# Kernel optimization log

Measured on AMD Instinct MI355X. Metric: run time of the kernel, lower is better.

Reference implementation:

```python
import jax, jax.numpy as jnp
import numpy as np

HEAD, SIZE = 16, 64
DIM = HEAD * SIZE
NINF = -10000.0
EPS = 1e-6


def setup_inputs() -> dict:
    key = jax.random.key(0)
    ks = jax.random.split(key, 12)
    B, S = 4, 2048
    std = 0.02
    return {
        "x": jax.random.normal(ks[0], (B, S, DIM), jnp.float32),
        "mask": jax.random.randint(ks[1], (B, S), 0, 2, jnp.int32),
        "wq_w": jax.random.normal(ks[2], (DIM, DIM), jnp.float32) * std,
        "wq_b": jnp.zeros((DIM,), jnp.float32),
        "wk_w": jax.random.normal(ks[3], (DIM, DIM), jnp.float32) * std,
        "wk_b": jnp.zeros((DIM,), jnp.float32),
        "wv_w": jax.random.normal(ks[4], (DIM, DIM), jnp.float32) * std,
        "wv_b": jnp.zeros((DIM,), jnp.float32),
        "dense_w": jax.random.normal(ks[5], (DIM, DIM), jnp.float32) * std,
        "dense_b": jnp.zeros((DIM,), jnp.float32),
        "gamma": jnp.ones((DIM,), jnp.float32),
        "beta": jnp.zeros((DIM,), jnp.float32),
    }


def _split_heads(t):
    # [B, S, DIM] -> [B, H, S, size]
    B, S, _ = t.shape
    return t.reshape(B, S, HEAD, SIZE).transpose(0, 2, 1, 3)


def _layernorm(x, gamma, beta):
    mu = jnp.mean(x, axis=-1, keepdims=True)
    var = jnp.mean(jnp.square(x - mu), axis=-1, keepdims=True)
    return (x - mu) * jax.lax.rsqrt(var + EPS) * gamma + beta


def reference(x, mask, wq_w, wq_b, wk_w, wk_b, wv_w, wv_b, dense_w, dense_b, gamma, beta):
    B, S, _ = x.shape
    q = _split_heads(x @ wq_w + wq_b)
    k = _split_heads(x @ wk_w + wk_b)
    v = _split_heads(x @ wv_w + wv_b)
    # scores [B, H, S, S]
    scores = jnp.einsum("bhqd,bhkd->bhqk", q, k) / jnp.sqrt(jnp.float32(SIZE))
    scores = scores + mask.astype(jnp.float32)[:, None, None, :] * NINF
    attn = jax.nn.softmax(scores, axis=-1)
    ctx = jnp.einsum("bhqk,bhkd->bhqd", attn, v)  # [B, H, S, size]
    ctx = ctx.transpose(0, 2, 1, 3).reshape(B, S, DIM)
    out = _layernorm(x + (ctx @ dense_w + dense_b), gamma, beta)
    return out, attn
```

## Files before the change

### kernel.cpp

```cpp
#include <hip/hip_runtime.h>
#include <stdint.h>

#define NB 4
#define NS 2048
#define NH 16
#define HSZ 64
#define ND 1024
#define NM (NB*NS)
#define QSCALE 0.180336880f
#define MADD2 -14426.950409f

typedef unsigned short u16;
typedef unsigned int u32;
typedef __attribute__((ext_vector_type(4))) float f32x4;
typedef __attribute__((ext_vector_type(8))) __bf16 bf16x8;

static __device__ __forceinline__ u16 f2bf(float f){
  unsigned int x = __builtin_bit_cast(unsigned int, f);
  x += 0x7fffu + ((x >> 16) & 1u);
  return (u16)(x >> 16);
}
static __device__ __forceinline__ u16 f2bf_rz(float f){
  return (u16)(__builtin_bit_cast(unsigned int, f) >> 16);
}

#define GLDS16(gp, lp) __builtin_amdgcn_global_load_lds( \
    (const __attribute__((address_space(1))) void*)(gp),  \
    (__attribute__((address_space(3))) void*)(lp), 16, 0, 0)

__global__ __launch_bounds__(256) void k_cast(const float4* __restrict__ in,
                                              ushort4* __restrict__ out, int n4){
  int i = blockIdx.x*256 + threadIdx.x;
  if (i >= n4) return;
  float4 v = in[i];
  ushort4 o;
  o.x = f2bf(v.x); o.y = f2bf(v.y); o.z = f2bf(v.z); o.w = f2bf(v.w);
  out[i] = o;
}

__global__ __launch_bounds__(256) void k_transpose4(const float* __restrict__ wq,
    const float* __restrict__ wk, const float* __restrict__ wv,
    const float* __restrict__ wd, u16* __restrict__ wcat, u16* __restrict__ wdt){
  __shared__ float t[32][33];
  const int z = blockIdx.z;
  const float* in = (z==0) ? wq : (z==1) ? wk : (z==2) ? wv : wd;
  u16* out = (z<3) ? (wcat + (size_t)z*ND*ND) : wdt;
  int tx = threadIdx.x & 31, ty = threadIdx.x >> 5;
  int n0 = blockIdx.x*32, k0 = blockIdx.y*32;
  #pragma unroll
  for (int i=0;i<32;i+=8)
    t[ty+i][tx] = in[(size_t)(k0+ty+i)*ND + n0 + tx];
  __syncthreads();
  #pragma unroll
  for (int i=0;i<32;i+=8)
    out[(size_t)(n0+ty+i)*ND + k0 + tx] = f2bf(t[tx][ty+i]);
}

template<int EPI>
__global__ __launch_bounds__(256,2) void k_gemm(const u16* __restrict__ A,
    const u16* __restrict__ Bt, const float* __restrict__ b0,
    const float* __restrict__ b1, const float* __restrict__ b2,
    const float* __restrict__ resid, u16* __restrict__ Qo, u16* __restrict__ Ko,
    u16* __restrict__ Vto, float* __restrict__ Out){
  __shared__ u16 sAB[2][128*64];
  u16* sA = sAB[0];
  u16* sB = sAB[1];
  const int tid = threadIdx.x;
  const int wave = tid >> 6, lane = tid & 63;
  const int l15 = lane & 15, l4 = lane >> 4;
  const int m0 = blockIdx.x * 128, n0 = blockIdx.y * 128;
  const int wm = wave >> 1, wn = wave & 1;
  const f32x4 vz = {0.f,0.f,0.f,0.f};
  f32x4 acc[4][4];
  #pragma unroll
  for (int i=0;i<4;i++)
    #pragma unroll
    for (int j=0;j<4;j++) acc[i][j] = vz;

  for (int k0 = 0; k0 < 1024; k0 += 64){
    __syncthreads();
    #pragma unroll
    for (int t=0; t<4; t++){
      const int jb = (t*4 + wave)*64;
      const int j  = jb + lane;
      const int r = j >> 3, c = (j & 7) << 3;
      GLDS16(A  + (((size_t)(m0 + r)) << 10) + (size_t)(k0 + c), sA + jb*8);
      GLDS16(Bt + (((size_t)(n0 + r)) << 10) + (size_t)(k0 + c), sB + jb*8);
    }
    __syncthreads();
    #pragma unroll
    for (int kk=0; kk<64; kk+=32){
      bf16x8 af[4], bv[4];
      #pragma unroll
      for (int mi=0;mi<4;mi++)
        af[mi] = *(const bf16x8*)(const void*)(sA + (wm*64 + mi*16 + l15)*64 + kk + l4*8);
      #pragma unroll
      for (int ni=0;ni<4;ni++)
        bv[ni] = *(const bf16x8*)(const void*)(sB + (wn*64 + ni*16 + l15)*64 + kk + l4*8);
      #pragma unroll
      for (int mi=0;mi<4;mi++)
        #pragma unroll
        for (int ni=0;ni<4;ni++)
          acc[mi][ni] = __builtin_amdgcn_mfma_f32_16x16x32_bf16(af[mi], bv[ni], acc[mi][ni], 0, 0, 0);
    }
  }

  if (EPI == 0){
    const int sec = n0 >> 10;
    const float* bias = (sec==0) ? b0 : (sec==1) ? b1 : b2;
    const float scale = (sec==0) ? QSCALE : 1.0f;
    if (sec < 2){
      u16* dst = (sec==0) ? Qo : Ko;
      #pragma unroll
      for (int mi=0;mi<4;mi++){
        #pragma unroll
        for (int ni=0;ni<4;ni++){
          const int n = n0 + wn*64 + ni*16 + l15;
          const int nn = n & (ND-1);
          const int h = nn >> 6, d = nn & 63;
          const float bvv = bias[nn];
          #pragma unroll
          for (int j=0;j<4;j++){
            const int m = m0 + wm*64 + mi*16 + l4*4 + j;
            const int b = m >> 11, s = m & (NS-1);
            const float v = (acc[mi][ni][j] + bvv) * scale;
            dst[((((size_t)b*NH + h)*NS + s) << 6) + d] = f2bf(v);
          }
        }
      }
    } else {
      __syncthreads();
      u16 (*sT)[128] = (u16(*)[128])sAB;
      #pragma unroll
      for (int mi=0;mi<4;mi++){
        #pragma unroll
        for (int ni=0;ni<4;ni++){
          const int nl = wn*64 + ni*16 + l15;
          const float bvv = bias[(n0 & (ND-1)) + nl];
          #pragma unroll
          for (int j=0;j<4;j++){
            const int ml = wm*64 + mi*16 + l4*4 + j;
            sT[nl][ml] = f2bf(acc[mi][ni][j] + bvv);
          }
        }
      }
      __syncthreads();
      const int nbase = n0 & (ND-1);
      const int b2 = m0 >> 11;
      const int sbase = m0 & (NS-1);
      #pragma unroll
      for (int it=0; it<8; ++it){
        const int idx = it*256 + tid;
        const int row = idx >> 4;
        const int ch  = (idx & 15) << 3;
        const int nn2 = nbase + row;
        const int h2 = nn2 >> 6, d2 = nn2 & 63;
        *(int4*)(void*)(Vto + ((((size_t)b2*NH + h2)*HSZ + d2) << 11) + sbase + ch)
            = *(const int4*)(const void*)&sT[row][ch];
      }
    }
  } else {
    #pragma unroll
    for (int mi=0;mi<4;mi++){
      #pragma unroll
      for (int ni=0;ni<4;ni++){
        const int n = n0 + wn*64 + ni*16 + l15;
        const float bvv = b0[n];
        #pragma unroll
        for (int j=0;j<4;j++){
          const int m = m0 + wm*64 + mi*16 + l4*4 + j;
          const size_t o = ((size_t)m << 10) + n;
          Out[o] = acc[mi][ni][j] + bvv + resid[o];
        }
      }
    }
  }
}

static __device__ __forceinline__ void attn_decode(int bid, int& qb, int& bh){
  const int x = bid & 7, t = bid >> 3;
  qb = t & 15;
  bh = (t >> 4) * 8 + x;
}
static __device__ __forceinline__ void attn_decode8(int bid, int& qb, int& bh){
  const int x = bid & 7, t = bid >> 3;
  qb = t & 7;
  bh = (t >> 3) * 8 + x;
}

__global__ __launch_bounds__(512,4) void k_attn_stats(const u16* __restrict__ Q,
    const u16* __restrict__ K, const int* __restrict__ mask,
    float* __restrict__ stats){
  __shared__ u16 sK[2][64][72];
  __shared__ float sMadd[NS];
  const int tid = threadIdx.x, wave = tid>>6, lane = tid&63;
  const int l15 = lane&15, l4 = lane>>4;
  int qb, bh; attn_decode8(blockIdx.x, qb, bh);
  const int b = bh >> 4;
  const size_t hoff = (size_t)bh * NS * HSZ;
  const int q0 = qb*256 + wave*32;
  const u16* Kg = K + hoff;
  bf16x8 qf0[2], qf1[2];
  #pragma unroll
  for (int m=0;m<2;m++){
    qf0[m] = *(const bf16x8*)(const void*)(Q + hoff + (size_t)(q0+m*16+l15)*HSZ + l4*8);
    qf1[m] = *(const bf16x8*)(const void*)(Q + hoff + (size_t)(q0+m*16+l15)*HSZ + 32 + l4*8);
  }
  const f32x4 vz = {0.f,0.f,0.f,0.f};
  const int r = tid >> 3, c = (tid & 7) << 3;
  float lr[2][4] = {{0.f,0.f,0.f,0.f},{0.f,0.f,0.f,0.f}};

  #pragma unroll
  for (int t=0;t<4;t++){
    const int kk = t*512 + tid;
    sMadd[kk] = mask[b*NS + kk] ? MADD2 : 0.f;
  }
  int4 rK = *(const int4*)(const void*)(Kg + (size_t)r*HSZ + c);
  *(int4*)(void*)&sK[0][r][c] = rK;
  rK = *(const int4*)(const void*)(Kg + (size_t)(64+r)*HSZ + c);
  __syncthreads();

  for (int kb=0; kb<NS; kb+=64){
    const int cur = (kb>>6)&1;
    if (kb+64 < NS)
      *(int4*)(void*)&sK[cur^1][r][c] = rK;
    if (kb+128 < NS)
      rK = *(const int4*)(const void*)(Kg + (size_t)(kb+128+r)*HSZ + c);
    #pragma unroll
    for (int n=0;n<4;n++){
      bf16x8 kf0 = *(const bf16x8*)(const void*)&sK[cur][n*16+l15][l4*8];
      bf16x8 kf1 = *(const bf16x8*)(const void*)&sK[cur][n*16+l15][32+l4*8];
      const float madd = sMadd[kb + n*16 + l15];
      #pragma unroll
      for (int m=0;m<2;m++){
        f32x4 a = vz;
        a = __builtin_amdgcn_mfma_f32_16x16x32_bf16(qf0[m], kf0, a, 0,0,0);
        a = __builtin_amdgcn_mfma_f32_16x16x32_bf16(qf1[m], kf1, a, 0,0,0);
        #pragma unroll
        for (int j=0;j<4;j++)
          lr[m][j] += __builtin_amdgcn_exp2f(a[j] + madd);
      }
    }
    __syncthreads();
  }
  #pragma unroll
  for (int m=0;m<2;m++)
    #pragma unroll
    for (int j=0;j<4;j++){
      float l = lr[m][j];
      #pragma unroll
      for (int off=1; off<16; off<<=1)
        l += __shfl_xor(l, off, 64);
      if (l15 == 0)
        stats[(size_t)bh*NS + q0 + m*16 + l4*4 + j] = 1.f/l;
    }
}

__global__ __launch_bounds__(512,4) void k_attn_pv(const u16* __restrict__ Q,
    const u16* __restrict__ K, const u16* __restrict__ Vt,
    const int* __restrict__ mask, const float* __restrict__ stats,
    float* __restrict__ attn, u16* __restrict__ ctx){
  __shared__ u16 sK[2][64][72];
  __shared__ u16 sV[2][64][72];
  __shared__ u16 sP[8][16][72];
  __shared__ float sMadd[NS];
  const int tid = threadIdx.x, wave = tid>>6, lane = tid&63;
  const int l15 = lane&15, l4 = lane>>4;
  int qb, bh; attn_decode(blockIdx.x, qb, bh);
  const int b = bh >> 4, h = bh & 15;
  const size_t hoff = (size_t)bh * NS * HSZ;
  const int q0 = qb*128 + wave*16;
  const u16* Kg = K + hoff;
  const u16* Vg = Vt + hoff;
  const bf16x8 qf0 = *(const bf16x8*)(const void*)(Q + hoff + (size_t)(q0+l15)*HSZ + l4*8);
  const bf16x8 qf1 = *(const bf16x8*)(const void*)(Q + hoff + (size_t)(q0+l15)*HSZ + 32 + l4*8);
  float rinv[4];
  #pragma unroll
  for (int j=0;j<4;j++)
    rinv[j] = stats[(size_t)bh*NS + q0 + l4*4 + j];
  const f32x4 vz = {0.f,0.f,0.f,0.f};
  f32x4 cacc[4];
  #pragma unroll
  for (int i=0;i<4;i++) cacc[i] = vz;
  float* attn_base = attn + (size_t)bh * NS * NS;
  const int r = tid >> 3, c = (tid & 7) << 3;

  #pragma unroll
  for (int t=0;t<4;t++){
    const int kk = t*512 + tid;
    sMadd[kk] = mask[b*NS + kk] ? MADD2 : 0.f;
  }
  int4 rK = *(const int4*)(const void*)(Kg + (size_t)r*HSZ + c);
  int4 rV = *(const int4*)(const void*)(Vg + (size_t)r*NS + c);
  *(int4*)(void*)&sK[0][r][c] = rK;
  *(int4*)(void*)&sV[0][r][c] = rV;
  rK = *(const int4*)(const void*)(Kg + (size_t)(64+r)*HSZ + c);
  rV = *(const int4*)(const void*)(Vg + (size_t)r*NS + 64 + c);
  __syncthreads();

  for (int kb=0; kb<NS; kb+=64){
    const int cur = (kb>>6)&1;
    if (kb+64 < NS){
      *(int4*)(void*)&sK[cur^1][r][c] = rK;
      *(int4*)(void*)&sV[cur^1][r][c] = rV;
    }
    if (kb+128 < NS){
      rK = *(const int4*)(const void*)(Kg + (size_t)(kb+128+r)*HSZ + c);
      rV = *(const int4*)(const void*)(Vg + (size_t)r*NS + (kb+128) + c);
    }
    #pragma unroll
    for (int n=0;n<4;n++){
      bf16x8 kf0 = *(const bf16x8*)(const void*)&sK[cur][n*16+l15][l4*8];
      bf16x8 kf1 = *(const bf16x8*)(const void*)&sK[cur][n*16+l15][32+l4*8];
      f32x4 a = vz;
      a = __builtin_amdgcn_mfma_f32_16x16x32_bf16(qf0, kf0, a, 0,0,0);
      a = __builtin_amdgcn_mfma_f32_16x16x32_bf16(qf1, kf1, a, 0,0,0);
      const float madd = sMadd[kb + n*16 + l15];
      #pragma unroll
      for (int j=0;j<4;j++){
        const float e = __builtin_amdgcn_exp2f(a[j] + madd);
        sP[wave][l4*4+j][n*16+l15] = f2bf_rz(e * rinv[j]);
      }
    }
    #pragma unroll
    for (int kk=0;kk<2;kk++){
      bf16x8 pf = *(const bf16x8*)(const void*)&sP[wave][l15][kk*32 + l4*8];
      #pragma unroll
      for (int n2=0;n2<4;n2++){
        bf16x8 vf = *(const bf16x8*)(const void*)&sV[cur][n2*16+l15][kk*32 + l4*8];
        cacc[n2] = __builtin_amdgcn_mfma_f32_16x16x32_bf16(pf, vf, cacc[n2], 0,0,0);
      }
    }
    #pragma unroll
    for (int jj=0;jj<4;jj++){
      const int rr = jj*4 + l4;
      const uint2 pw = *(const uint2*)(const void*)&sP[wave][rr][l15*4];
      f32x4 o;
      o.x = __builtin_bit_cast(float, pw.x << 16);
      o.y = __builtin_bit_cast(float, pw.x & 0xffff0000u);
      o.z = __builtin_bit_cast(float, pw.y << 16);
      o.w = __builtin_bit_cast(float, pw.y & 0xffff0000u);
      __builtin_nontemporal_store(o,
          (f32x4*)(void*)&attn_base[(size_t)(q0 + rr)*NS + kb + l15*4]);
    }
    __syncthreads();
  }
  #pragma unroll
  for (int n2=0;n2<4;n2++)
    #pragma unroll
    for (int j=0;j<4;j++){
      const int q = q0 + l4*4 + j;
      ctx[(((size_t)(b*NS + q)) << 10) + h*HSZ + n2*16 + l15] = f2bf(cacc[n2][j]);
    }
}

__global__ __launch_bounds__(256) void k_layernorm(float* __restrict__ buf,
    const float* __restrict__ gamma, const float* __restrict__ beta){
  const int row = blockIdx.x, tid = threadIdx.x;
  float4* rp = (float4*)(buf + ((size_t)row << 10));
  float4 a = rp[tid];
  float s  = a.x + a.y + a.z + a.w;
  float ss = a.x*a.x + a.y*a.y + a.z*a.z + a.w*a.w;
  #pragma unroll
  for (int off=1; off<64; off<<=1){
    s  += __shfl_xor(s,  off, 64);
    ss += __shfl_xor(ss, off, 64);
  }
  __shared__ float red[8];
  const int wave = tid>>6, lane = tid&63;
  if (lane == 0){ red[wave] = s; red[wave+4] = ss; }
  __syncthreads();
  s  = red[0]+red[1]+red[2]+red[3];
  ss = red[4]+red[5]+red[6]+red[7];
  const float mu  = s * (1.f/1024.f);
  const float var = ss * (1.f/1024.f) - mu*mu;
  const float rs  = rsqrtf(var + 1e-6f);
  float4 g  = ((const float4*)gamma)[tid];
  float4 be = ((const float4*)beta)[tid];
  f32x4 o;
  o.x = (a.x-mu)*rs*g.x + be.x;
  o.y = (a.y-mu)*rs*g.y + be.y;
  o.z = (a.z-mu)*rs*g.z + be.z;
  o.w = (a.w-mu)*rs*g.w + be.w;
  __builtin_nontemporal_store(o, (f32x4*)(void*)&rp[tid]);
}

extern "C" void kernel_launch(void* const* d_in, const int* in_sizes, int n_in,
                              void* d_out, int out_size, void* d_ws, size_t ws_size,
                              hipStream_t stream){
  const float* x     = (const float*)d_in[0];
  const int*   mask  = (const int*)d_in[1];
  const float* wq_w  = (const float*)d_in[2];
  const float* wq_b  = (const float*)d_in[3];
  const float* wk_w  = (const float*)d_in[4];
  const float* wk_b  = (const float*)d_in[5];
  const float* wv_w  = (const float*)d_in[6];
  const float* wv_b  = (const float*)d_in[7];
  const float* wd_w  = (const float*)d_in[8];
  const float* wd_b  = (const float*)d_in[9];
  const float* gamma = (const float*)d_in[10];
  const float* beta  = (const float*)d_in[11];

  float* out0 = (float*)d_out;
  float* attn = out0 + (size_t)NM * ND;

  char* ws = (char*)d_ws;
  u16*   xb    = (u16*)(ws);
  u16*   ctx   = (u16*)(ws);
  u16*   wcat  = (u16*)(ws + (16u<<20));
  u16*   wdt   = (u16*)(ws + (22u<<20));
  u16*   Qb    = (u16*)(ws + (24u<<20));
  u16*   Kb    = (u16*)(ws + (40u<<20));
  u16*   Vtb   = (u16*)(ws + (56u<<20));
  float* stats = (float*)(ws + (72u<<20));

  k_cast<<<8192, 256, 0, stream>>>((const float4*)x, (ushort4*)xb, NM*ND/4);
  k_transpose4<<<dim3(32,32,4), 256, 0, stream>>>(wq_w, wk_w, wv_w, wd_w, wcat, wdt);

  k_gemm<0><<<dim3(64,24), 256, 0, stream>>>(xb, wcat, wq_b, wk_b, wv_b,
                                             nullptr, Qb, Kb, Vtb, nullptr);

  k_attn_stats<<<512, 512, 0, stream>>>(Qb, Kb, mask, stats);
  k_attn_pv<<<1024, 512, 0, stream>>>(Qb, Kb, Vtb, mask, stats, attn, ctx);

  k_gemm<2><<<dim3(64,8), 256, 0, stream>>>(ctx, wdt, wd_b, nullptr, nullptr,
                                            x, nullptr, nullptr, nullptr, out0);
  k_layernorm<<<NM, 256, 0, stream>>>(out0, gamma, beta);
}
```

Measured before the change: 397.6 us.

## Fuse attention row-sum statistics pass into the PV kernel

Removes the separate stats kernel and computes the softmax denominators inside the PV kernel with a first sweep over K, then reuses them for the normalized attention write and PV accumulation. This drops one launch and the stats buffer round trip. Each block now handles 16 query rows per wave rather than 32 in the stats pass, so K is streamed through shared memory twice per block and the QK^T work for the stats is done at lower reuse.

```diff
diff --git a/kernel.cpp b/kernel.cpp
--- a/kernel.cpp
+++ b/kernel.cpp
@@ -182,84 +182,10 @@
   qb = t & 15;
   bh = (t >> 4) * 8 + x;
 }
-static __device__ __forceinline__ void attn_decode8(int bid, int& qb, int& bh){
-  const int x = bid & 7, t = bid >> 3;
-  qb = t & 7;
-  bh = (t >> 3) * 8 + x;
-}
-
-__global__ __launch_bounds__(512,4) void k_attn_stats(const u16* __restrict__ Q,
-    const u16* __restrict__ K, const int* __restrict__ mask,
-    float* __restrict__ stats){
-  __shared__ u16 sK[2][64][72];
-  __shared__ float sMadd[NS];
-  const int tid = threadIdx.x, wave = tid>>6, lane = tid&63;
-  const int l15 = lane&15, l4 = lane>>4;
-  int qb, bh; attn_decode8(blockIdx.x, qb, bh);
-  const int b = bh >> 4;
-  const size_t hoff = (size_t)bh * NS * HSZ;
-  const int q0 = qb*256 + wave*32;
-  const u16* Kg = K + hoff;
-  bf16x8 qf0[2], qf1[2];
-  #pragma unroll
-  for (int m=0;m<2;m++){
-    qf0[m] = *(const bf16x8*)(const void*)(Q + hoff + (size_t)(q0+m*16+l15)*HSZ + l4*8);
-    qf1[m] = *(const bf16x8*)(const void*)(Q + hoff + (size_t)(q0+m*16+l15)*HSZ + 32 + l4*8);
-  }
-  const f32x4 vz = {0.f,0.f,0.f,0.f};
-  const int r = tid >> 3, c = (tid & 7) << 3;
-  float lr[2][4] = {{0.f,0.f,0.f,0.f},{0.f,0.f,0.f,0.f}};
-
-  #pragma unroll
-  for (int t=0;t<4;t++){
-    const int kk = t*512 + tid;
-    sMadd[kk] = mask[b*NS + kk] ? MADD2 : 0.f;
-  }
-  int4 rK = *(const int4*)(const void*)(Kg + (size_t)r*HSZ + c);
-  *(int4*)(void*)&sK[0][r][c] = rK;
-  rK = *(const int4*)(const void*)(Kg + (size_t)(64+r)*HSZ + c);
-  __syncthreads();
-
-  for (int kb=0; kb<NS; kb+=64){
-    const int cur = (kb>>6)&1;
-    if (kb+64 < NS)
-      *(int4*)(void*)&sK[cur^1][r][c] = rK;
-    if (kb+128 < NS)
-      rK = *(const int4*)(const void*)(Kg + (size_t)(kb+128+r)*HSZ + c);
-    #pragma unroll
-    for (int n=0;n<4;n++){
-      bf16x8 kf0 = *(const bf16x8*)(const void*)&sK[cur][n*16+l15][l4*8];
-      bf16x8 kf1 = *(const bf16x8*)(const void*)&sK[cur][n*16+l15][32+l4*8];
-      const float madd = sMadd[kb + n*16 + l15];
-      #pragma unroll
-      for (int m=0;m<2;m++){
-        f32x4 a = vz;
-        a = __builtin_amdgcn_mfma_f32_16x16x32_bf16(qf0[m], kf0, a, 0,0,0);
-        a = __builtin_amdgcn_mfma_f32_16x16x32_bf16(qf1[m], kf1, a, 0,0,0);
-        #pragma unroll
-        for (int j=0;j<4;j++)
-          lr[m][j] += __builtin_amdgcn_exp2f(a[j] + madd);
-      }
-    }
-    __syncthreads();
-  }
-  #pragma unroll
-  for (int m=0;m<2;m++)
-    #pragma unroll
-    for (int j=0;j<4;j++){
-      float l = lr[m][j];
-      #pragma unroll
-      for (int off=1; off<16; off<<=1)
-        l += __shfl_xor(l, off, 64);
-      if (l15 == 0)
-        stats[(size_t)bh*NS + q0 + m*16 + l4*4 + j] = 1.f/l;
-    }
-}
-
-__global__ __launch_bounds__(512,4) void k_attn_pv(const u16* __restrict__ Q,
+
+__global__ __launch_bounds__(512,4) void k_attn_fused(const u16* __restrict__ Q,
     const u16* __restrict__ K, const u16* __restrict__ Vt,
-    const int* __restrict__ mask, const float* __restrict__ stats,
-    float* __restrict__ attn, u16* __restrict__ ctx){
+    const int* __restrict__ mask, float* __restrict__ attn, u16* __restrict__ ctx){
   __shared__ u16 sK[2][64][72];
   __shared__ u16 sV[2][64][72];
   __shared__ u16 sP[8][16][72];
@@ -274,15 +200,7 @@
   const u16* Vg = Vt + hoff;
   const bf16x8 qf0 = *(const bf16x8*)(const void*)(Q + hoff + (size_t)(q0+l15)*HSZ + l4*8);
   const bf16x8 qf1 = *(const bf16x8*)(const void*)(Q + hoff + (size_t)(q0+l15)*HSZ + 32 + l4*8);
-  float rinv[4];
-  #pragma unroll
-  for (int j=0;j<4;j++)
-    rinv[j] = stats[(size_t)bh*NS + q0 + l4*4 + j];
   const f32x4 vz = {0.f,0.f,0.f,0.f};
-  f32x4 cacc[4];
-  #pragma unroll
-  for (int i=0;i<4;i++) cacc[i] = vz;
-  float* attn_base = attn + (size_t)bh * NS * NS;
   const int r = tid >> 3, c = (tid & 7) << 3;
 
   #pragma unroll
@@ -290,6 +208,49 @@
     const int kk = t*512 + tid;
     sMadd[kk] = mask[b*NS + kk] ? MADD2 : 0.f;
   }
+
+  float lr[4] = {0.f,0.f,0.f,0.f};
+  {
+    int4 rK = *(const int4*)(const void*)(Kg + (size_t)r*HSZ + c);
+    *(int4*)(void*)&sK[0][r][c] = rK;
+    rK = *(const int4*)(const void*)(Kg + (size_t)(64+r)*HSZ + c);
+    __syncthreads();
+    for (int kb=0; kb<NS; kb+=64){
+      const int cur = (kb>>6)&1;
+      if (kb+64 < NS)
+        *(int4*)(void*)&sK[cur^1][r][c] = rK;
+      if (kb+128 < NS)
+        rK = *(const int4*)(const void*)(Kg + (size_t)(kb+128+r)*HSZ + c);
+      #pragma unroll
+      for (int n=0;n<4;n++){
+        bf16x8 kf0 = *(const bf16x8*)(const void*)&sK[cur][n*16+l15][l4*8];
+        bf16x8 kf1 = *(const bf16x8*)(const void*)&sK[cur][n*16+l15][32+l4*8];
+        f32x4 a = vz;
+        a = __builtin_amdgcn_mfma_f32_16x16x32_bf16(qf0, kf0, a, 0,0,0);
+        a = __builtin_amdgcn_mfma_f32_16x16x32_bf16(qf1, kf1, a, 0,0,0);
+        const float madd = sMadd[kb + n*16 + l15];
+        #pragma unroll
+        for (int j=0;j<4;j++)
+          lr[j] += __builtin_amdgcn_exp2f(a[j] + madd);
+      }
+      __syncthreads();
+    }
+  }
+  float rinv[4];
+  #pragma unroll
+  for (int j=0;j<4;j++){
+    float l = lr[j];
+    #pragma unroll
+    for (int off=1; off<16; off<<=1)
+      l += __shfl_xor(l, off, 64);
+    rinv[j] = 1.f/l;
+  }
+
+  f32x4 cacc[4];
+  #pragma unroll
+  for (int i=0;i<4;i++) cacc[i] = vz;
+  float* attn_base = attn + (size_t)bh * NS * NS;
+
   int4 rK = *(const int4*)(const void*)(Kg + (size_t)r*HSZ + c);
   int4 rV = *(const int4*)(const void*)(Vg + (size_t)r*NS + c);
   *(int4*)(void*)&sK[0][r][c] = rK;
@@ -412,7 +373,6 @@
   u16*   Qb    = (u16*)(ws + (24u<<20));
   u16*   Kb    = (u16*)(ws + (40u<<20));
   u16*   Vtb   = (u16*)(ws + (56u<<20));
-  float* stats = (float*)(ws + (72u<<20));
 
   k_cast<<<8192, 256, 0, stream>>>((const float4*)x, (ushort4*)xb, NM*ND/4);
   k_transpose4<<<dim3(32,32,4), 256, 0, stream>>>(wq_w, wk_w, wv_w, wd_w, wcat, wdt);
@@ -420,8 +380,7 @@
   k_gemm<0><<<dim3(64,24), 256, 0, stream>>>(xb, wcat, wq_b, wk_b, wv_b,
                                              nullptr, Qb, Kb, Vtb, nullptr);
 
-  k_attn_stats<<<512, 512, 0, stream>>>(Qb, Kb, mask, stats);
-  k_attn_pv<<<1024, 512, 0, stream>>>(Qb, Kb, Vtb, mask, stats, attn, ctx);
+  k_attn_fused<<<1024, 512, 0, stream>>>(Qb, Kb, Vtb, mask, attn, ctx);
 
   k_gemm<2><<<dim3(64,8), 256, 0, stream>>>(ctx, wdt, wd_b, nullptr, nullptr,
                                             x, nullptr, nullptr, nullptr, out0);
```

Measured after the change: 365.9 us. -8.0%, faster.
